# Kernel tuning notes

Measured on AMD Instinct MI355X. Metric: run time of the kernel, lower is better.

## Reference

```python
import jax, jax.numpy as jnp
import numpy as np

NUM_GRAPHS = 64
NEG_SLOPE_EDGE = 0.2   # GATLayer alpha
NEG_SLOPE_READ = 0.01  # torch default leaky_relu slope in ReadoutLayer


def leaky_relu(x, slope):
    return jnp.where(x >= 0, x, slope * x)


def segment_softmax(e, seg, n):
    # numerically stable softmax of edge logits grouped by destination node
    m = jax.ops.segment_max(e, seg, num_segments=n)
    m = jnp.where(jnp.isfinite(m), m, 0.0)  # guard nodes with no in-edges
    ex = jnp.exp(e - m[seg])
    s = jax.ops.segment_sum(ex, seg, num_segments=n)
    return ex / jnp.where(s > 0, s, 1.0)[seg]


def gat_layer(h, src, dst, e_feat, W, a):
    n = h.shape[0]
    out = W.shape[1]
    z = h @ W                                      # [N, out]
    a_src, a_dst, a_e = a[:out], a[out:2 * out], a[2 * out:]
    # concat([z_src, z_dst, e_feat]) @ a  ==  z_src@a_src + z_dst@a_dst + e@a_e
    logits = leaky_relu(z[src] @ a_src + z[dst] @ a_dst + e_feat @ a_e,
                        NEG_SLOPE_EDGE)            # [E]
    alpha = segment_softmax(logits, dst, n)        # [E]
    msg = alpha[:, None] * z[src]                  # [E, out]
    return jax.ops.segment_sum(msg, dst, num_segments=n)  # [N, out]


def readout(h, gid, w_att, b_att):
    # DGL mean_nodes(g, 'z', 'att'): multiply feat by weight, then mean per graph
    att = jnp.exp(leaky_relu(h @ w_att + b_att, NEG_SLOPE_READ))  # [N]
    num = jax.ops.segment_sum(att[:, None] * h, gid, num_segments=NUM_GRAPHS)
    cnt = jax.ops.segment_sum(jnp.ones_like(att), gid, num_segments=NUM_GRAPHS)
    return num / jnp.maximum(cnt, 1.0)[:, None]    # [G, hidden]


def setup_inputs() -> dict:
    key = jax.random.key(0)
    ks = jax.random.split(key, 16)
    N, E, F_IN, H, ED, C = 50000, 800000, 128, 128, 16, 10
    sc = lambda f: np.float32(1.0 / np.sqrt(f))
    return {
        "x": jax.random.normal(ks[0], (N, F_IN), jnp.float32),
        "e_feat": jax.random.normal(ks[1], (E, ED), jnp.float32),
        "src": jax.random.randint(ks[2], (E,), 0, N, dtype=jnp.int32),
        "dst": jax.random.randint(ks[3], (E,), 0, N, dtype=jnp.int32),
        "gid": jnp.sort(jax.random.randint(ks[4], (N,), 0, NUM_GRAPHS, dtype=jnp.int32)),
        "W1": jax.random.normal(ks[5], (F_IN, H), jnp.float32) * sc(F_IN),
        "a1": jax.random.normal(ks[6], (2 * H + ED,), jnp.float32) * sc(2 * H + ED),
        "W2": jax.random.normal(ks[7], (H, H), jnp.float32) * sc(H),
        "a2": jax.random.normal(ks[8], (2 * H + ED,), jnp.float32) * sc(2 * H + ED),
        "W3": jax.random.normal(ks[9], (H, H), jnp.float32) * sc(H),
        "a3": jax.random.normal(ks[10], (2 * H + ED,), jnp.float32) * sc(2 * H + ED),
        "w_att": jax.random.normal(ks[11], (H,), jnp.float32) * sc(H),
        "b_att": jnp.zeros((), jnp.float32),
        "W_cls": jax.random.normal(ks[12], (3 * H, C), jnp.float32) * sc(3 * H),
        "b_cls": jnp.zeros((C,), jnp.float32),
    }


def reference(x, e_feat, src, dst, gid, W1, a1, W2, a2, W3, a3,
              w_att, b_att, W_cls, b_cls):
    # dropout is identity at inference (training=False)
    h1 = jax.nn.relu(gat_layer(x, src, dst, e_feat, W1, a1))
    hg1 = readout(h1, gid, w_att, b_att)
    h2 = jax.nn.relu(gat_layer(h1, src, dst, e_feat, W2, a2))
    hg2 = readout(h2, gid, w_att, b_att)
    h3 = jax.nn.relu(gat_layer(h2, src, dst, e_feat, W3, a3))
    hg3 = readout(h3, gid, w_att, b_att)
    y = jnp.concatenate([hg1, hg2, hg3], axis=1) @ W_cls + b_cls  # [G, C]
    return jax.nn.log_softmax(y, axis=1)
```

## Files before the change

### kernel.cpp

```cpp
#include <hip/hip_runtime.h>
#include <math.h>

#define HD 128
#define ED 16
#define NG 64
#define NC 10

typedef short bf16x8 __attribute__((ext_vector_type(8)));
typedef float f32x4 __attribute__((ext_vector_type(4)));

__device__ __forceinline__ unsigned short f2b(float x){
  unsigned u = __float_as_uint(x);
  unsigned r = (u + 0x7fffu + ((u >> 16) & 1u)) >> 16;
  return (unsigned short)r;
}
__device__ __forceinline__ float blo(unsigned p){ return __uint_as_float(p << 16); }
__device__ __forceinline__ float bhi(unsigned p){ return __uint_as_float(p & 0xffff0000u); }
__device__ __forceinline__ float bperm_f(int idx, float v){
  return __int_as_float(__builtin_amdgcn_ds_bpermute(idx<<2, __float_as_int(v)));
}
__device__ __forceinline__ int bperm_i(int idx, int v){
  return __builtin_amdgcn_ds_bpermute(idx<<2, v);
}

__global__ void k_hist(const int* __restrict__ dst, int* __restrict__ deg,
                       int* __restrict__ rank, int E){
  int e4 = (blockIdx.x*blockDim.x + threadIdx.x)*4;
  if(e4+3 < E){
    int4 d = *(const int4*)&dst[e4];
    int4 r;
    r.x = atomicAdd(&deg[d.x], 1);
    r.y = atomicAdd(&deg[d.y], 1);
    r.z = atomicAdd(&deg[d.z], 1);
    r.w = atomicAdd(&deg[d.w], 1);
    *(int4*)&rank[e4] = r;
  } else {
    for(int k=0;k<4;k++) if(e4+k<E) rank[e4+k] = atomicAdd(&deg[dst[e4+k]], 1);
  }
}

__global__ __launch_bounds__(64) void k_bsum(const int* __restrict__ deg, int* __restrict__ bsum, int N){
  int b = blockIdx.x, t = threadIdx.x;
  int i = b*256 + t*4;
  int s = 0;
  if(i+3 < N){ int4 v = *(const int4*)&deg[i]; s = v.x+v.y+v.z+v.w; }
  else { for(int k=0;k<4;k++) if(i+k<N) s += deg[i+k]; }
  #pragma unroll
  for(int o=32;o;o>>=1) s += __shfl_xor(s,o);
  if(t==0) bsum[b] = s;
}

__global__ __launch_bounds__(1024) void k_bscan(const int* __restrict__ bsum, int* __restrict__ bbase,
                                                int* __restrict__ offs, int N, int nb){
  __shared__ int sh[1024];
  int t = threadIdx.x;
  int v = (t < nb) ? bsum[t] : 0;
  sh[t] = v; __syncthreads();
  for(int o=1;o<1024;o<<=1){ int u = (t>=o)?sh[t-o]:0; __syncthreads(); sh[t]+=u; __syncthreads(); }
  if(t < nb) bbase[t] = sh[t] - v;
  if(t == 1023) offs[N] = sh[1023];
}

__global__ __launch_bounds__(256) void k_bprop(const int* __restrict__ deg, const int* __restrict__ bbase,
                                               int* __restrict__ offs, int N){
  __shared__ int sh[256];
  int b = blockIdx.x, t = threadIdx.x;
  int i = b*256 + t;
  int v = (i<N) ? deg[i] : 0;
  sh[t] = v; __syncthreads();
  for(int o=1;o<256;o<<=1){ int u = (t>=o)?sh[t-o]:0; __syncthreads(); sh[t]+=u; __syncthreads(); }
  if(i<N){ offs[i] = bbase[b] + sh[t] - v; }
}

__global__ __launch_bounds__(256) void k_scatterq(const int* __restrict__ src, const int* __restrict__ dst,
                           const int* __restrict__ rank,
                           const float* __restrict__ ef,
                           const float* __restrict__ a1e, const float* __restrict__ a2e,
                           const float* __restrict__ a3e,
                           const int* __restrict__ offs, uint2* __restrict__ rec, int E){
  int t = blockIdx.x*256 + threadIdx.x;
  int e = t >> 2;
  int sub = t & 3;
  if(e >= E) return;
  float4 f  = *(const float4*)&ef[(size_t)e*ED + sub*4];
  float4 A1 = *(const float4*)&a1e[sub*4];
  float4 A2 = *(const float4*)&a2e[sub*4];
  float4 A3 = *(const float4*)&a3e[sub*4];
  float q1 = fmaf(f.x,A1.x, fmaf(f.y,A1.y, fmaf(f.z,A1.z, f.w*A1.w)));
  float q2 = fmaf(f.x,A2.x, fmaf(f.y,A2.y, fmaf(f.z,A2.z, f.w*A2.w)));
  float q3 = fmaf(f.x,A3.x, fmaf(f.y,A3.y, fmaf(f.z,A3.z, f.w*A3.w)));
  q1 += __shfl_xor(q1,1); q1 += __shfl_xor(q1,2);
  q2 += __shfl_xor(q2,1); q2 += __shfl_xor(q2,2);
  q3 += __shfl_xor(q3,1); q3 += __shfl_xor(q3,2);
  if(sub == 0){
    int d = dst[e];
    int p = offs[d] + rank[e];
    uint2 A;
    A.x = (unsigned)f2b(q1) | ((unsigned)f2b(q2) << 16);
    A.y = (unsigned)src[e] | ((unsigned)f2b(q3) << 16);
    rec[p] = A;
  }
}

__global__ __launch_bounds__(256) void k_setup(const float* __restrict__ x, unsigned short* __restrict__ xb,
                        const float* __restrict__ W1, const float* __restrict__ W2,
                        const float* __restrict__ W3, unsigned short* __restrict__ Wb,
                        const int* __restrict__ gid, float* __restrict__ cnt,
                        int N, int ncast){
  int b = blockIdx.x;
  if(b < ncast){
    int i = (b*256 + threadIdx.x)*8;
    if(i >= N*HD) return;
    float4 v0 = *(const float4*)&x[i];
    float4 v1 = *(const float4*)&x[i+4];
    uint4 o;
    o.x = f2b(v0.x) | ((unsigned)f2b(v0.y)<<16);
    o.y = f2b(v0.z) | ((unsigned)f2b(v0.w)<<16);
    o.z = f2b(v1.x) | ((unsigned)f2b(v1.y)<<16);
    o.w = f2b(v1.z) | ((unsigned)f2b(v1.w)<<16);
    *(uint4*)&xb[i] = o;
  } else if(b < ncast + 24){
    int idx = (b - ncast)*256 + threadIdx.x;
    if(idx >= 3*2048) return;
    int layer = idx >> 11;
    int r = idx & 2047;
    const float* W = (layer==0)?W1:((layer==1)?W2:W3);
    int lane = r & 63, tile = r >> 6;
    int kt = tile >> 3, nt = tile & 7;
    int qq = lane >> 4, cc = lane & 15;
    int kbase = kt*32 + qq*8;
    int col = nt*16 + cc;
    unsigned short tmp[8];
    #pragma unroll
    for(int j=0;j<8;j++) tmp[j] = f2b(W[(size_t)(kbase+j)*HD + col]);
    uint4 o;
    o.x = tmp[0]|((unsigned)tmp[1]<<16); o.y = tmp[2]|((unsigned)tmp[3]<<16);
    o.z = tmp[4]|((unsigned)tmp[5]<<16); o.w = tmp[6]|((unsigned)tmp[7]<<16);
    *(uint4*)&Wb[(size_t)idx*8] = o;
  } else {
    int g = threadIdx.x;
    if(g >= NG) return;
    int lo=0, hi=N;
    while(lo<hi){ int mid=(lo+hi)>>1; if(gid[mid] < g) lo=mid+1; else hi=mid; }
    int start = lo; lo = start; hi = N;
    while(lo<hi){ int mid=(lo+hi)>>1; if(gid[mid] < g+1) lo=mid+1; else hi=mid; }
    cnt[g] = (float)(lo - start);
  }
}

__global__ __launch_bounds__(256) void k_gemm_mfma(
    const unsigned short* __restrict__ Ab,
    const unsigned short* __restrict__ Wb,
    unsigned short* __restrict__ Zb,
    const float* __restrict__ avec,
    float* __restrict__ ps, float* __restrict__ pd, int M)
{
  int tid = threadIdx.x;
  int w = tid >> 6, lane = tid & 63;
  int q = lane >> 4, c = lane & 15;
  int rowbase = blockIdx.x*128 + w*32;
  f32x4 acc[2][8];
  #pragma unroll
  for(int t=0;t<2;t++)
    #pragma unroll
    for(int n=0;n<8;n++) acc[t][n] = (f32x4){0.f,0.f,0.f,0.f};

  int r0 = rowbase + c;      if(r0 > M-1) r0 = M-1;
  int r1 = rowbase + 16 + c; if(r1 > M-1) r1 = M-1;
  #pragma unroll
  for(int kt=0; kt<4; kt++){
    int ko = kt*32 + q*8;
    bf16x8 a0 = __builtin_bit_cast(bf16x8, *(const uint4*)&Ab[(size_t)r0*HD + ko]);
    bf16x8 a1 = __builtin_bit_cast(bf16x8, *(const uint4*)&Ab[(size_t)r1*HD + ko]);
    #pragma unroll
    for(int n=0;n<8;n++){
      bf16x8 b = __builtin_bit_cast(bf16x8, *(const uint4*)&Wb[(((size_t)(kt*8+n))*64 + lane)*8]);
      acc[0][n] = __builtin_amdgcn_mfma_f32_16x16x32_bf16(a0, b, acc[0][n], 0,0,0);
      acc[1][n] = __builtin_amdgcn_mfma_f32_16x16x32_bf16(a1, b, acc[1][n], 0,0,0);
    }
  }
  float asv[8], adv[8];
  #pragma unroll
  for(int n=0;n<8;n++){ asv[n] = avec[n*16+c]; adv[n] = avec[HD + n*16+c]; }
  #pragma unroll
  for(int t=0;t<2;t++){
    #pragma unroll
    for(int r=0;r<4;r++){
      int grow = rowbase + t*16 + 4*q + r;
      bool ok = grow < M;
      #pragma unroll
      for(int n=0;n<8;n++){
        if(ok) Zb[(size_t)grow*HD + n*16 + c] = f2b(acc[t][n][r]);
      }
      float pp = 0.f, dd = 0.f;
      #pragma unroll
      for(int n=0;n<8;n++){ pp = fmaf(acc[t][n][r], asv[n], pp); dd = fmaf(acc[t][n][r], adv[n], dd); }
      #pragma unroll
      for(int o=1;o<16;o<<=1){ pp += __shfl_xor(pp,o); dd += __shfl_xor(dd,o); }
      if(ok && c==0){ ps[grow] = pp; pd[grow] = dd; }
    }
  }
}

__global__ __launch_bounds__(256) void k_agg2(const uint4* __restrict__ zb4,
                                              const int* __restrict__ offs,
                                              const uint2* __restrict__ rec,
                                              const float* __restrict__ ps,
                                              const float* __restrict__ pd,
                                              int layer,
                                              unsigned* __restrict__ hbu,
                                              float* __restrict__ att,
                                              const float* __restrict__ watt,
                                              const float* __restrict__ batt, int N){
  int wid = blockIdx.x*4 + (threadIdx.x>>6);
  int lane = threadIdx.x & 63;
  if(wid >= N) return;
  int q = lane >> 4, c = lane & 15;
  int d0 = offs[wid], d1 = offs[wid+1];
  float pdv = pd[wid];
  float acc[8];
  #pragma unroll
  for(int i=0;i<8;i++) acc[i]=0.f;
  float ssum = 0.f;

  for(int t0=d0; t0<d1; t0+=64){
    int rem = d1 - t0; if(rem > 64) rem = 64;
    int j = t0 + lane;
    float w = 0.f; int u = 0;
    if(j < d1){
      uint2 R = rec[j];
      u = (int)(R.y & 0xffffu);
      unsigned qb = (layer==0) ? (R.x & 0xffffu) : (layer==1 ? (R.x >> 16) : (R.y >> 16));
      float ql = __uint_as_float(qb << 16);
      float l = ps[u] + pdv + ql;
      l = (l >= 0.f) ? l : 0.2f*l;
      w = __expf(l);
    }
    float ws = w;
    #pragma unroll
    for(int o=32;o;o>>=1) ws += __shfl_xor(ws,o);
    ssum += ws;
    for(int jb=0; jb<rem; jb+=16){
      float w0 = bperm_f(jb+q,    w);  int u0 = bperm_i(jb+q,    u);
      float w1 = bperm_f(jb+4+q,  w);  int u1 = bperm_i(jb+4+q,  u);
      float w2 = bperm_f(jb+8+q,  w);  int u2 = bperm_i(jb+8+q,  u);
      float w3 = bperm_f(jb+12+q, w);  int u3 = bperm_i(jb+12+q, u);
      uint4 P0 = zb4[(size_t)u0*16 + c];
      uint4 P1 = zb4[(size_t)u1*16 + c];
      uint4 P2 = zb4[(size_t)u2*16 + c];
      uint4 P3 = zb4[(size_t)u3*16 + c];
      acc[0] = fmaf(w0, blo(P0.x), acc[0]); acc[1] = fmaf(w0, bhi(P0.x), acc[1]);
      acc[2] = fmaf(w0, blo(P0.y), acc[2]); acc[3] = fmaf(w0, bhi(P0.y), acc[3]);
      acc[4] = fmaf(w0, blo(P0.z), acc[4]); acc[5] = fmaf(w0, bhi(P0.z), acc[5]);
      acc[6] = fmaf(w0, blo(P0.w), acc[6]); acc[7] = fmaf(w0, bhi(P0.w), acc[7]);
      acc[0] = fmaf(w1, blo(P1.x), acc[0]); acc[1] = fmaf(w1, bhi(P1.x), acc[1]);
      acc[2] = fmaf(w1, blo(P1.y), acc[2]); acc[3] = fmaf(w1, bhi(P1.y), acc[3]);
      acc[4] = fmaf(w1, blo(P1.z), acc[4]); acc[5] = fmaf(w1, bhi(P1.z), acc[5]);
      acc[6] = fmaf(w1, blo(P1.w), acc[6]); acc[7] = fmaf(w1, bhi(P1.w), acc[7]);
      acc[0] = fmaf(w2, blo(P2.x), acc[0]); acc[1] = fmaf(w2, bhi(P2.x), acc[1]);
      acc[2] = fmaf(w2, blo(P2.y), acc[2]); acc[3] = fmaf(w2, bhi(P2.y), acc[3]);
      acc[4] = fmaf(w2, blo(P2.z), acc[4]); acc[5] = fmaf(w2, bhi(P2.z), acc[5]);
      acc[6] = fmaf(w2, blo(P2.w), acc[6]); acc[7] = fmaf(w2, bhi(P2.w), acc[7]);
      acc[0] = fmaf(w3, blo(P3.x), acc[0]); acc[1] = fmaf(w3, bhi(P3.x), acc[1]);
      acc[2] = fmaf(w3, blo(P3.y), acc[2]); acc[3] = fmaf(w3, bhi(P3.y), acc[3]);
      acc[4] = fmaf(w3, blo(P3.z), acc[4]); acc[5] = fmaf(w3, bhi(P3.z), acc[5]);
      acc[6] = fmaf(w3, blo(P3.w), acc[6]); acc[7] = fmaf(w3, bhi(P3.w), acc[7]);
    }
  }
  #pragma unroll
  for(int i=0;i<8;i++){ acc[i] += __shfl_xor(acc[i],16); acc[i] += __shfl_xor(acc[i],32); }
  float inv = (d1 > d0) ? 1.0f/ssum : 0.0f;
  #pragma unroll
  for(int i=0;i<8;i++) acc[i] = fmaxf(acc[i]*inv, 0.f);
  hbu[(size_t)wid*64 + c*4 + q] = (unsigned)f2b(acc[2*q]) | ((unsigned)f2b(acc[2*q+1])<<16);
  float4 w0v = *(const float4*)&watt[c*8];
  float4 w1v = *(const float4*)&watt[c*8+4];
  float t = acc[0]*w0v.x + acc[1]*w0v.y + acc[2]*w0v.z + acc[3]*w0v.w
          + acc[4]*w1v.x + acc[5]*w1v.y + acc[6]*w1v.z + acc[7]*w1v.w;
  #pragma unroll
  for(int o=1;o<16;o<<=1) t += __shfl_xor(t,o);
  t += batt[0];
  float lr = (t >= 0.f) ? t : 0.01f*t;
  if(lane==0) att[wid] = __expf(lr);
}

#define RCH 16
__global__ __launch_bounds__(64) void k_readout(const unsigned* __restrict__ hbu,
                                                const float* __restrict__ att,
                                                const int* __restrict__ gid,
                                                float* __restrict__ hg, int N){
  int g = blockIdx.x / RCH;
  int chunk = blockIdx.x % RCH;
  int t = threadIdx.x;
  int lo=0, hi=N;
  while(lo<hi){ int mid=(lo+hi)>>1; if(gid[mid] < g) lo=mid+1; else hi=mid; }
  int start = lo; lo = start; hi = N;
  while(lo<hi){ int mid=(lo+hi)>>1; if(gid[mid] < g+1) lo=mid+1; else hi=mid; }
  int end = lo;
  int len = end - start;
  int c0 = start + (int)(((long long)len * chunk) / RCH);
  int c1 = start + (int)(((long long)len * (chunk+1)) / RCH);
  float acc0 = 0.f, acc1 = 0.f;
  for(int v=c0; v<c1; v++){
    unsigned P = hbu[(size_t)v*64 + t];
    float a = att[v];
    acc0 = fmaf(a, blo(P), acc0);
    acc1 = fmaf(a, bhi(P), acc1);
  }
  atomicAdd(&hg[g*HD + 2*t],     acc0);
  atomicAdd(&hg[g*HD + 2*t + 1], acc1);
}

__global__ __launch_bounds__(384) void k_final(const float* __restrict__ hg,
                                               const float* __restrict__ cnt,
                                               const float* __restrict__ Wc,
                                               const float* __restrict__ bc,
                                               float* __restrict__ out){
  int g = blockIdx.x;
  int t = threadIdx.x;
  __shared__ float red[6];
  __shared__ float yv[NC];
  float invc = 1.f / fmaxf(cnt[g], 1.f);
  int part = t >> 7;
  int f = t & 127;
  float v = hg[(size_t)part*NG*HD + g*HD + f] * invc;
  for(int c=0; c<NC; c++){
    float p = v * Wc[(size_t)t*NC + c];
    #pragma unroll
    for(int o=32;o;o>>=1) p += __shfl_xor(p,o);
    if((t&63)==0) red[t>>6] = p;
    __syncthreads();
    if(t==0) yv[c] = bc[c] + red[0]+red[1]+red[2]+red[3]+red[4]+red[5];
    __syncthreads();
  }
  if(t==0){
    float mx = -INFINITY;
    #pragma unroll
    for(int c=0;c<NC;c++) mx = fmaxf(mx, yv[c]);
    float s = 0.f;
    #pragma unroll
    for(int c=0;c<NC;c++) s += __expf(yv[c] - mx);
    float ls = logf(s);
    #pragma unroll
    for(int c=0;c<NC;c++) out[g*NC + c] = yv[c] - mx - ls;
  }
}

extern "C" void kernel_launch(void* const* d_in, const int* in_sizes, int n_in,
                              void* d_out, int out_size, void* d_ws, size_t ws_size,
                              hipStream_t stream) {
  const float* x     = (const float*)d_in[0];
  const float* efeat = (const float*)d_in[1];
  const int*   src   = (const int*)d_in[2];
  const int*   dst   = (const int*)d_in[3];
  const int*   gid   = (const int*)d_in[4];
  const float* W1    = (const float*)d_in[5];
  const float* a1    = (const float*)d_in[6];
  const float* W2    = (const float*)d_in[7];
  const float* a2    = (const float*)d_in[8];
  const float* W3    = (const float*)d_in[9];
  const float* a3    = (const float*)d_in[10];
  const float* watt  = (const float*)d_in[11];
  const float* batt  = (const float*)d_in[12];
  const float* Wc    = (const float*)d_in[13];
  const float* bc    = (const float*)d_in[14];
  float* out = (float*)d_out;

  int N = in_sizes[4];
  int E = in_sizes[2];

  char* p = (char*)d_ws;
  auto alloc = [&](size_t bytes)->void*{
    void* r = (void*)p;
    p += (bytes + 255) & ~(size_t)255;
    return r;
  };
  unsigned short* Xb = (unsigned short*)alloc((size_t)N*HD*2);
  unsigned short* Hb = (unsigned short*)alloc((size_t)N*HD*2);
  unsigned short* Zb = (unsigned short*)alloc((size_t)N*HD*2);
  unsigned short* Wball = (unsigned short*)alloc((size_t)3*2048*8*2);
  float* ps      = (float*)alloc((size_t)N*4);
  float* pd      = (float*)alloc((size_t)N*4);
  float* att     = (float*)alloc((size_t)N*4);
  int*   deg     = (int*)  alloc((size_t)N*4);
  int*   offs    = (int*)  alloc((size_t)(N+1)*4);
  int*   rank    = (int*)  alloc((size_t)E*4);
  uint2* rec     = (uint2*)alloc((size_t)E*8);
  int*   bsum    = (int*)  alloc((size_t)1024*4);
  int*   bbase   = (int*)  alloc((size_t)1024*4);
  float* hg      = (float*)alloc((size_t)3*NG*HD*4);
  float* cnt     = (float*)alloc((size_t)NG*4);
  (void)ws_size; (void)n_in; (void)out_size;

  int nwblocks = (N + 3) / 4;
  int nb = (N + 255) / 256;
  int ncast = (N*16 + 255) / 256;

  hipMemsetAsync(deg, 0, (size_t)N*4, stream);
  hipMemsetAsync(hg, 0, (size_t)3*NG*HD*4, stream);
  k_hist<<<(E/4 + 255)/256, 256, 0, stream>>>(dst, deg, rank, E);
  k_bsum<<<nb, 64, 0, stream>>>(deg, bsum, N);
  k_bscan<<<1, 1024, 0, stream>>>(bsum, bbase, offs, N, nb);
  k_bprop<<<nb, 256, 0, stream>>>(deg, bbase, offs, N);
  k_scatterq<<<(E*4 + 255)/256, 256, 0, stream>>>(src, dst, rank, efeat,
                                                  a1+2*HD, a2+2*HD, a3+2*HD,
                                                  offs, rec, E);
  k_setup<<<ncast + 25, 256, 0, stream>>>(x, Xb, W1, W2, W3, Wball, gid, cnt, N, ncast);

  const float* as[3] = {a1, a2, a3};
  for(int layer=0; layer<3; layer++){
    const unsigned short* Ab = (layer==0) ? Xb : Hb;
    k_gemm_mfma<<<(N+127)/128, 256, 0, stream>>>(Ab, Wball + (size_t)layer*2048*8, Zb,
                                                 as[layer], ps, pd, N);
    k_agg2<<<nwblocks, 256, 0, stream>>>((const uint4*)Zb, offs, rec, ps, pd, layer,
                                         (unsigned*)Hb, att, watt, batt, N);
    k_readout<<<NG*RCH, 64, 0, stream>>>((const unsigned*)Hb, att, gid,
                                         hg + (size_t)layer*NG*HD, N);
  }
  k_final<<<NG, 384, 0, stream>>>(hg, cnt, Wc, bc, out);
}
```

Baseline: 432.2 us.

## Fuse preprocessing, scan, scatter and readout with per-layer GEMMs to cut launches

Several independent stages now share one launch through block-index dispatch. The degree histogram, x/W bf16 casts, graph counts and zeroing of hg are merged into one kernel. The single-block scan is removed: each prefix block now sums all earlier block totals itself. The edge-record scatter shares a launch with the layer-1 GEMM, and each layer's readout shares a launch with the next layer's GEMM. This is meant to cut launch overhead and serialization between small kernels, and to let independent work overlap. In exchange, the prefix computation is redundant, and heterogeneous blocks in one grid may balance unevenly.

```diff
diff --git a/kernel.cpp b/kernel.cpp
--- a/kernel.cpp
+++ b/kernel.cpp
@@ -23,20 +23,77 @@
   return __builtin_amdgcn_ds_bpermute(idx<<2, v);
 }
 
-__global__ void k_hist(const int* __restrict__ dst, int* __restrict__ deg,
-                       int* __restrict__ rank, int E){
-  int e4 = (blockIdx.x*blockDim.x + threadIdx.x)*4;
-  if(e4+3 < E){
-    int4 d = *(const int4*)&dst[e4];
-    int4 r;
-    r.x = atomicAdd(&deg[d.x], 1);
-    r.y = atomicAdd(&deg[d.y], 1);
-    r.z = atomicAdd(&deg[d.z], 1);
-    r.w = atomicAdd(&deg[d.w], 1);
-    *(int4*)&rank[e4] = r;
-  } else {
-    for(int k=0;k<4;k++) if(e4+k<E) rank[e4+k] = atomicAdd(&deg[dst[e4+k]], 1);
-  }
+__global__ __launch_bounds__(256) void k_pre(
+    const int* __restrict__ dst, int* __restrict__ deg, int* __restrict__ rank, int E, int NH,
+    const float* __restrict__ x, unsigned short* __restrict__ xb,
+    const float* __restrict__ W1, const float* __restrict__ W2, const float* __restrict__ W3,
+    unsigned short* __restrict__ Wb,
+    const int* __restrict__ gid, float* __restrict__ cnt,
+    float* __restrict__ hg,
+    int N, int ncast){
+  int b = blockIdx.x;
+  if(b < NH){
+    int e4 = (b*256 + threadIdx.x)*4;
+    if(e4+3 < E){
+      int4 d = *(const int4*)&dst[e4];
+      int4 r;
+      r.x = atomicAdd(&deg[d.x], 1);
+      r.y = atomicAdd(&deg[d.y], 1);
+      r.z = atomicAdd(&deg[d.z], 1);
+      r.w = atomicAdd(&deg[d.w], 1);
+      *(int4*)&rank[e4] = r;
+    } else {
+      for(int k=0;k<4;k++) if(e4+k<E) rank[e4+k] = atomicAdd(&deg[dst[e4+k]], 1);
+    }
+    return;
+  }
+  b -= NH;
+  if(b < ncast){
+    int i = (b*256 + threadIdx.x)*8;
+    if(i >= N*HD) return;
+    float4 v0 = *(const float4*)&x[i];
+    float4 v1 = *(const float4*)&x[i+4];
+    uint4 o;
+    o.x = f2b(v0.x) | ((unsigned)f2b(v0.y)<<16);
+    o.y = f2b(v0.z) | ((unsigned)f2b(v0.w)<<16);
+    o.z = f2b(v1.x) | ((unsigned)f2b(v1.y)<<16);
+    o.w = f2b(v1.z) | ((unsigned)f2b(v1.w)<<16);
+    *(uint4*)&xb[i] = o;
+    return;
+  }
+  b -= ncast;
+  if(b < 24){
+    int idx = b*256 + threadIdx.x;
+    if(idx >= 3*2048) return;
+    int layer = idx >> 11;
+    int r = idx & 2047;
+    const float* W = (layer==0)?W1:((layer==1)?W2:W3);
+    int lane = r & 63, tile = r >> 6;
+    int kt = tile >> 3, nt = tile & 7;
+    int qq = lane >> 4, cc = lane & 15;
+    int kbase = kt*32 + qq*8;
+    int col = nt*16 + cc;
+    unsigned short tmp[8];
+    #pragma unroll
+    for(int j=0;j<8;j++) tmp[j] = f2b(W[(size_t)(kbase+j)*HD + col]);
+    uint4 o;
+    o.x = tmp[0]|((unsigned)tmp[1]<<16); o.y = tmp[2]|((unsigned)tmp[3]<<16);
+    o.z = tmp[4]|((unsigned)tmp[5]<<16); o.w = tmp[6]|((unsigned)tmp[7]<<16);
+    *(uint4*)&Wb[(size_t)idx*8] = o;
+    return;
+  }
+  if(b == 24){
+    int g = threadIdx.x;
+    if(g >= NG) return;
+    int lo=0, hi=N;
+    while(lo<hi){ int mid=(lo+hi)>>1; if(gid[mid] < g) lo=mid+1; else hi=mid; }
+    int start = lo; lo = start; hi = N;
+    while(lo<hi){ int mid=(lo+hi)>>1; if(gid[mid] < g+1) lo=mid+1; else hi=mid; }
+    cnt[g] = (float)(lo - start);
+    return;
+  }
+  int i = ((b-25)*256 + threadIdx.x)*4;
+  *(float4*)&hg[i] = (float4){0.f,0.f,0.f,0.f};
 }
 
 __global__ __launch_bounds__(64) void k_bsum(const int* __restrict__ deg, int* __restrict__ bsum, int N){
@@ -50,35 +107,39 @@
   if(t==0) bsum[b] = s;
 }
 
-__global__ __launch_bounds__(1024) void k_bscan(const int* __restrict__ bsum, int* __restrict__ bbase,
-                                                int* __restrict__ offs, int N, int nb){
-  __shared__ int sh[1024];
-  int t = threadIdx.x;
-  int v = (t < nb) ? bsum[t] : 0;
-  sh[t] = v; __syncthreads();
-  for(int o=1;o<1024;o<<=1){ int u = (t>=o)?sh[t-o]:0; __syncthreads(); sh[t]+=u; __syncthreads(); }
-  if(t < nb) bbase[t] = sh[t] - v;
-  if(t == 1023) offs[N] = sh[1023];
-}
-
-__global__ __launch_bounds__(256) void k_bprop(const int* __restrict__ deg, const int* __restrict__ bbase,
-                                               int* __restrict__ offs, int N){
+__global__ __launch_bounds__(256) void k_bprop2(const int* __restrict__ deg,
+                                                const int* __restrict__ bsum,
+                                                int* __restrict__ offs, int N, int E){
   __shared__ int sh[256];
+  __shared__ int sbase;
   int b = blockIdx.x, t = threadIdx.x;
+  int s = 0;
+  for(int j=t; j<b; j+=256) s += bsum[j];
+  #pragma unroll
+  for(int o=32;o;o>>=1) s += __shfl_xor(s,o);
+  if(t < 4) sh[t] = 0;
+  __syncthreads();
+  if((t&63)==0) sh[t>>6] = s;
+  __syncthreads();
+  if(t==0) sbase = sh[0]+sh[1]+sh[2]+sh[3];
+  __syncthreads();
   int i = b*256 + t;
   int v = (i<N) ? deg[i] : 0;
   sh[t] = v; __syncthreads();
   for(int o=1;o<256;o<<=1){ int u = (t>=o)?sh[t-o]:0; __syncthreads(); sh[t]+=u; __syncthreads(); }
-  if(i<N){ offs[i] = bbase[b] + sh[t] - v; }
-}
-
-__global__ __launch_bounds__(256) void k_scatterq(const int* __restrict__ src, const int* __restrict__ dst,
+  if(i<N) offs[i] = sbase + sh[t] - v;
+  if(b==0 && t==0) offs[N] = E;
+}
+
+
+__device__ __forceinline__ void scatter_dev(int bidx,
+                           const int* __restrict__ src, const int* __restrict__ dst,
                            const int* __restrict__ rank,
                            const float* __restrict__ ef,
                            const float* __restrict__ a1e, const float* __restrict__ a2e,
                            const float* __restrict__ a3e,
                            const int* __restrict__ offs, uint2* __restrict__ rec, int E){
-  int t = blockIdx.x*256 + threadIdx.x;
+  int t = bidx*256 + threadIdx.x;
   int e = t >> 2;
   int sub = t & 3;
   if(e >= E) return;
@@ -102,53 +163,7 @@
   }
 }
 
-__global__ __launch_bounds__(256) void k_setup(const float* __restrict__ x, unsigned short* __restrict__ xb,
-                        const float* __restrict__ W1, const float* __restrict__ W2,
-                        const float* __restrict__ W3, unsigned short* __restrict__ Wb,
-                        const int* __restrict__ gid, float* __restrict__ cnt,
-                        int N, int ncast){
-  int b = blockIdx.x;
-  if(b < ncast){
-    int i = (b*256 + threadIdx.x)*8;
-    if(i >= N*HD) return;
-    float4 v0 = *(const float4*)&x[i];
-    float4 v1 = *(const float4*)&x[i+4];
-    uint4 o;
-    o.x = f2b(v0.x) | ((unsigned)f2b(v0.y)<<16);
-    o.y = f2b(v0.z) | ((unsigned)f2b(v0.w)<<16);
-    o.z = f2b(v1.x) | ((unsigned)f2b(v1.y)<<16);
-    o.w = f2b(v1.z) | ((unsigned)f2b(v1.w)<<16);
-    *(uint4*)&xb[i] = o;
-  } else if(b < ncast + 24){
-    int idx = (b - ncast)*256 + threadIdx.x;
-    if(idx >= 3*2048) return;
-    int layer = idx >> 11;
-    int r = idx & 2047;
-    const float* W = (layer==0)?W1:((layer==1)?W2:W3);
-    int lane = r & 63, tile = r >> 6;
-    int kt = tile >> 3, nt = tile & 7;
-    int qq = lane >> 4, cc = lane & 15;
-    int kbase = kt*32 + qq*8;
-    int col = nt*16 + cc;
-    unsigned short tmp[8];
-    #pragma unroll
-    for(int j=0;j<8;j++) tmp[j] = f2b(W[(size_t)(kbase+j)*HD + col]);
-    uint4 o;
-    o.x = tmp[0]|((unsigned)tmp[1]<<16); o.y = tmp[2]|((unsigned)tmp[3]<<16);
-    o.z = tmp[4]|((unsigned)tmp[5]<<16); o.w = tmp[6]|((unsigned)tmp[7]<<16);
-    *(uint4*)&Wb[(size_t)idx*8] = o;
-  } else {
-    int g = threadIdx.x;
-    if(g >= NG) return;
-    int lo=0, hi=N;
-    while(lo<hi){ int mid=(lo+hi)>>1; if(gid[mid] < g) lo=mid+1; else hi=mid; }
-    int start = lo; lo = start; hi = N;
-    while(lo<hi){ int mid=(lo+hi)>>1; if(gid[mid] < g+1) lo=mid+1; else hi=mid; }
-    cnt[g] = (float)(lo - start);
-  }
-}
-
-__global__ __launch_bounds__(256) void k_gemm_mfma(
+__device__ __forceinline__ void gemm_dev(int bidx,
     const unsigned short* __restrict__ Ab,
     const unsigned short* __restrict__ Wb,
     unsigned short* __restrict__ Zb,
@@ -158,7 +173,7 @@
   int tid = threadIdx.x;
   int w = tid >> 6, lane = tid & 63;
   int q = lane >> 4, c = lane & 15;
-  int rowbase = blockIdx.x*128 + w*32;
+  int rowbase = bidx*128 + w*32;
   f32x4 acc[2][8];
   #pragma unroll
   for(int t=0;t<2;t++)
@@ -200,6 +215,55 @@
       if(ok && c==0){ ps[grow] = pp; pd[grow] = dd; }
     }
   }
+}
+
+#define RCH 16
+__device__ __forceinline__ void readout_dev(int rb,
+                          const unsigned* __restrict__ hbu,
+                          const float* __restrict__ att,
+                          const int* __restrict__ gid,
+                          float* __restrict__ hg, int N){
+  int g = rb >> 2;
+  int chunk = ((rb & 3) << 2) + (threadIdx.x >> 6);
+  int t = threadIdx.x & 63;
+  int lo=0, hi=N;
+  while(lo<hi){ int mid=(lo+hi)>>1; if(gid[mid] < g) lo=mid+1; else hi=mid; }
+  int start = lo; lo = start; hi = N;
+  while(lo<hi){ int mid=(lo+hi)>>1; if(gid[mid] < g+1) lo=mid+1; else hi=mid; }
+  int end = lo;
+  int len = end - start;
+  int c0 = start + (int)(((long long)len * chunk) / RCH);
+  int c1 = start + (int)(((long long)len * (chunk+1)) / RCH);
+  float acc0 = 0.f, acc1 = 0.f;
+  for(int v=c0; v<c1; v++){
+    unsigned P = hbu[(size_t)v*64 + t];
+    float a = att[v];
+    acc0 = fmaf(a, blo(P), acc0);
+    acc1 = fmaf(a, bhi(P), acc1);
+  }
+  atomicAdd(&hg[g*HD + 2*t],     acc0);
+  atomicAdd(&hg[g*HD + 2*t + 1], acc1);
+}
+
+__global__ __launch_bounds__(256) void k_sg1(
+    const unsigned short* __restrict__ Ab, const unsigned short* __restrict__ Wb,
+    unsigned short* __restrict__ Zb, const float* __restrict__ avec,
+    float* __restrict__ ps, float* __restrict__ pd, int M, int GB,
+    const int* __restrict__ src, const int* __restrict__ dst, const int* __restrict__ rank,
+    const float* __restrict__ ef, const float* __restrict__ a1e, const float* __restrict__ a2e,
+    const float* __restrict__ a3e, const int* __restrict__ offs, uint2* __restrict__ rec, int E){
+  if(blockIdx.x < GB) gemm_dev(blockIdx.x, Ab, Wb, Zb, avec, ps, pd, M);
+  else scatter_dev(blockIdx.x - GB, src, dst, rank, ef, a1e, a2e, a3e, offs, rec, E);
+}
+
+__global__ __launch_bounds__(256) void k_rg(
+    const unsigned short* __restrict__ Ab, const unsigned short* __restrict__ Wb,
+    unsigned short* __restrict__ Zb, const float* __restrict__ avec,
+    float* __restrict__ ps, float* __restrict__ pd, int M, int GB,
+    const unsigned* __restrict__ hbu, const float* __restrict__ att,
+    const int* __restrict__ gid, float* __restrict__ hg, int N){
+  if(blockIdx.x < GB) gemm_dev(blockIdx.x, Ab, Wb, Zb, avec, ps, pd, M);
+  else readout_dev(blockIdx.x - GB, hbu, att, gid, hg, N);
 }
 
 __global__ __launch_bounds__(256) void k_agg2(const uint4* __restrict__ zb4,
@@ -284,7 +348,6 @@
   if(lane==0) att[wid] = __expf(lr);
 }
 
-#define RCH 16
 __global__ __launch_bounds__(64) void k_readout(const unsigned* __restrict__ hbu,
                                                 const float* __restrict__ att,
                                                 const int* __restrict__ gid,
@@ -387,7 +450,6 @@
   int*   rank    = (int*)  alloc((size_t)E*4);
   uint2* rec     = (uint2*)alloc((size_t)E*8);
   int*   bsum    = (int*)  alloc((size_t)1024*4);
-  int*   bbase   = (int*)  alloc((size_t)1024*4);
   float* hg      = (float*)alloc((size_t)3*NG*HD*4);
   float* cnt     = (float*)alloc((size_t)NG*4);
   (void)ws_size; (void)n_in; (void)out_size;
@@ -395,27 +457,30 @@
   int nwblocks = (N + 3) / 4;
   int nb = (N + 255) / 256;
   int ncast = (N*16 + 255) / 256;
+  int NH = (E/4 + 255) / 256;
+  int GB = (N + 127) / 128;
+  int SB = (E*4 + 255) / 256;
 
   hipMemsetAsync(deg, 0, (size_t)N*4, stream);
-  hipMemsetAsync(hg, 0, (size_t)3*NG*HD*4, stream);
-  k_hist<<<(E/4 + 255)/256, 256, 0, stream>>>(dst, deg, rank, E);
+  k_pre<<<NH + ncast + 49, 256, 0, stream>>>(dst, deg, rank, E, NH,
+                                             x, Xb, W1, W2, W3, Wball,
+                                             gid, cnt, hg, N, ncast);
   k_bsum<<<nb, 64, 0, stream>>>(deg, bsum, N);
-  k_bscan<<<1, 1024, 0, stream>>>(bsum, bbase, offs, N, nb);
-  k_bprop<<<nb, 256, 0, stream>>>(deg, bbase, offs, N);
-  k_scatterq<<<(E*4 + 255)/256, 256, 0, stream>>>(src, dst, rank, efeat,
-                                                  a1+2*HD, a2+2*HD, a3+2*HD,
-                                                  offs, rec, E);
-  k_setup<<<ncast + 25, 256, 0, stream>>>(x, Xb, W1, W2, W3, Wball, gid, cnt, N, ncast);
-
-  const float* as[3] = {a1, a2, a3};
-  for(int layer=0; layer<3; layer++){
-    const unsigned short* Ab = (layer==0) ? Xb : Hb;
-    k_gemm_mfma<<<(N+127)/128, 256, 0, stream>>>(Ab, Wball + (size_t)layer*2048*8, Zb,
-                                                 as[layer], ps, pd, N);
-    k_agg2<<<nwblocks, 256, 0, stream>>>((const uint4*)Zb, offs, rec, ps, pd, layer,
-                                         (unsigned*)Hb, att, watt, batt, N);
-    k_readout<<<NG*RCH, 64, 0, stream>>>((const unsigned*)Hb, att, gid,
-                                         hg + (size_t)layer*NG*HD, N);
-  }
+  k_bprop2<<<nb, 256, 0, stream>>>(deg, bsum, offs, N, E);
+  k_sg1<<<GB + SB, 256, 0, stream>>>(Xb, Wball, Zb, a1, ps, pd, N, GB,
+                                     src, dst, rank, efeat,
+                                     a1+2*HD, a2+2*HD, a3+2*HD, offs, rec, E);
+  k_agg2<<<nwblocks, 256, 0, stream>>>((const uint4*)Zb, offs, rec, ps, pd, 0,
+                                       (unsigned*)Hb, att, watt, batt, N);
+  k_rg<<<GB + NG*4, 256, 0, stream>>>(Hb, Wball + (size_t)1*2048*8, Zb, a2, ps, pd, N, GB,
+                                      (const unsigned*)Hb, att, gid, hg + 0*NG*HD, N);
+  k_agg2<<<nwblocks, 256, 0, stream>>>((const uint4*)Zb, offs, rec, ps, pd, 1,
+                                       (unsigned*)Hb, att, watt, batt, N);
+  k_rg<<<GB + NG*4, 256, 0, stream>>>(Hb, Wball + (size_t)2*2048*8, Zb, a3, ps, pd, N, GB,
+                                      (const unsigned*)Hb, att, gid, hg + 1*NG*HD, N);
+  k_agg2<<<nwblocks, 256, 0, stream>>>((const uint4*)Zb, offs, rec, ps, pd, 2,
+                                       (unsigned*)Hb, att, watt, batt, N);
+  k_readout<<<NG*RCH, 64, 0, stream>>>((const unsigned*)Hb, att, gid,
+                                       hg + 2*NG*HD, N);
   k_final<<<NG, 384, 0, stream>>>(hg, cnt, Wc, bc, out);
 }
```

Measured after the change: 415.1 us. 4.0% less time.
